# Kernel optimization log

Hardware: AMD Instinct MI355X
Metric: run time of the kernel (lower is better)

The kernel has to match this reference:

```python
import jax, jax.numpy as jnp
from jax import lax
import numpy as np

B, H, W = 8, 352, 1216
CLIPVARIANCE = 5.0   # init kwarg
MAXRANGE = 32        # init kwarg

# 1-pixel shifts with zero padding. out[...,m,n] = x at the shifted location.
def s_pos_w(x):  # out[..., n] = x[..., n-1]
    return jnp.pad(x[..., :, :-1], ((0, 0), (0, 0), (0, 0), (1, 0)))

def s_neg_w(x):  # out[..., n] = x[..., n+1]
    return jnp.pad(x[..., :, 1:], ((0, 0), (0, 0), (0, 0), (0, 1)))

def s_pos_h(x):  # out[..., m, :] = x[..., m-1, :]
    return jnp.pad(x[..., :-1, :], ((0, 0), (0, 0), (1, 0), (0, 0)))

def s_neg_h(x):  # out[..., m, :] = x[..., m+1, :]
    return jnp.pad(x[..., 1:, :], ((0, 0), (0, 0), (0, 1), (0, 0)))


def _dir_accumulate(shift, logstep, depthin, maskf, var_d):
    """Scan outward up to MAXRANGE steps in one direction, accumulating
    confidence weights exp(-min(var, clip)) and variance-weighted depth
    hypotheses depth[src] * exp(integrated log-gradient along the path).
    Paths break at the first unmasked pixel (valid is a running product)."""
    z = jnp.zeros_like(depthin)

    def body(carry, _):
        valid, c, dsh, vsh, aw, awd = carry
        valid = shift(valid * maskf)          # path contiguity
        c = logstep(c)                         # integrated log-depth ratio
        dsh = shift(dsh)                       # source-pixel depth
        vsh = shift(vsh)                       # source-pixel variance
        w = jnp.exp(-jnp.minimum(vsh, CLIPVARIANCE)) * valid
        aw = aw + w
        awd = awd + w * jnp.exp(c) * dsh
        return (valid, c, dsh, vsh, aw, awd), None

    init = (jnp.ones_like(depthin), z, depthin, var_d, z, z)
    (_, _, _, _, aw, awd), _ = lax.scan(body, init, None, length=MAXRANGE)
    return aw, awd


def crf_lateralre(pred_log, mask, variance, depthin):
    """One 4-direction variance-weighted CRF integration pass."""
    maskf = mask.astype(depthin.dtype)
    plog_h = pred_log[:, 0:1]  # log d[m,n+1] - log d[m,n]
    plog_v = pred_log[:, 1:2]  # log d[m+1,n] - log d[m,n]

    dirs = [
        (s_pos_w, lambda c: s_pos_w(c + plog_h), variance[:, 0:1]),  # from left
        (s_neg_w, lambda c: s_neg_w(c) - plog_h, variance[:, 1:2]),  # from right
        (s_pos_h, lambda c: s_pos_h(c + plog_v), variance[:, 2:3]),  # from above
        (s_neg_h, lambda c: s_neg_h(c) - plog_v, variance[:, 3:4]),  # from below
    ]

    tot_w = jnp.zeros_like(depthin)
    tot_wd = jnp.zeros_like(depthin)
    for shift, logstep, var_d in dirs:
        aw, awd = _dir_accumulate(shift, logstep, depthin, maskf, var_d)
        tot_w = tot_w + aw
        tot_wd = tot_wd + awd

    lateralre = jnp.where(tot_w > 0, tot_wd / jnp.maximum(tot_w, 1e-12), 0.0)
    return lateralre * maskf


def setup_inputs() -> dict:
    key = jax.random.key(0)
    k1, k2, k3, k4 = jax.random.split(key, 4)
    pred_log = jax.random.normal(k1, (B, 2, H, W), jnp.float32) * 0.05
    mask = (jax.random.uniform(k2, (B, 1, H, W)) < 0.9).astype(jnp.int32)
    variance = jax.random.uniform(k3, (B, 4, H, W), jnp.float32) * 8.0
    depthin = jax.random.uniform(k4, (B, 1, H, W), jnp.float32) * 10.0 + 1.0
    lam = jnp.array([0.2], jnp.float32)
    return {"pred_log": pred_log, "mask": mask, "variance": variance,
            "depthin": depthin, "lam": lam, "times": 1}


def reference(pred_log, mask, variance, depthin, lam, times):
    depthout = depthin
    for _ in range(times):
        lateralre = crf_lateralre(pred_log, mask, variance, depthout)
        sel = (lateralre > 0).astype(depthin.dtype)
        depthout = (1 - sel) * depthin + sel * (depthin * (1 - lam) + lateralre * lam)
    return depthout
```

## Files before the change

### kernel.cpp

```cpp
#include <hip/hip_runtime.h>
#include <stdint.h>

#define HH 352
#define WW 1216
#define HW (HH*WW)
#define BB 8
#define CLIPV 5.0f
#define MAXR 32

#define VR 22
#define NBAND (HH/VR)
#define PFD 12
#define TOT (VR + MAXR)

template<int DIR>
__device__ __forceinline__ void vert_scan(
    const int* __restrict__ m, const float* __restrict__ plog_v,
    const float* __restrict__ vp, const float* __restrict__ d,
    const int w, const int h0, const int lane,
    float2 (&obuf0)[VR][64], float (&obw)[VR], float (&obq)[VR])
{
    const int hs   = DIR ? (h0 + VR - 1 + MAXR) : (h0 - MAXR);
    const int step = DIR ? -1 : 1;

    float rq_q[VR], rq_w[VR];
    int   r_mi[PFD];
    float r_pl[PFD], r_vv[PFD], r_dd[PFD];

    #pragma unroll
    for (int p = 0; p < PFD; ++p) {
        int hp = hs + p * step;
        int hc = min(max(hp, 0), HH-1);
        int idx = hc * WW + w;
        r_mi[p] = m[idx];
        r_pl[p] = plog_v[idx];
        r_vv[p] = vp[idx];
        r_dd[p] = d[idx];
    }

    float Q = 0.f, W = 0.f, EG = 1.f;
    int last_inv = hs - step;

    #pragma unroll
    for (int it = 0; it < TOT; ++it) {
        const int h  = hs + it * step;
        const int sl = it % PFD;

        int   mi  = ((unsigned)h < (unsigned)HH) ? r_mi[sl] : 0;
        float pl  = r_pl[sl];
        float vvx = r_vv[sl];
        float dd  = r_dd[sl];

        if (it + PFD < TOT) {
            int hp = h + PFD * step;
            int hc = min(max(hp, 0), HH-1);
            int idx = hc * WW + w;
            r_mi[sl] = m[idx];
            r_pl[sl] = plog_v[idx];
            r_vv[sl] = vp[idx];
            r_dd[sl] = d[idx];
        }

        bool  res = (mi == 0);
        float g   = __expf(pl);
        float wt  = __expf(-fminf(vvx, CLIPV));
        float q, outw, outq;
        if constexpr (DIR == 0) {
            outw = W; outq = EG * Q;
            q = wt * dd * __builtin_amdgcn_rcpf(EG);
            Q  = res ? 0.f : (Q + q);
            W  = res ? 0.f : (W + wt);
            EG = res ? 1.f : (EG * g);
        } else {
            float EDh = EG * g;
            outw = W; outq = Q * __builtin_amdgcn_rcpf(EDh);
            q = wt * dd * EDh;
            Q  = res ? 0.f : (Q + q);
            W  = res ? 0.f : (W + wt);
            EG = res ? 1.f : EDh;
        }
        last_inv = res ? h : last_inv;

        if (it >= MAXR) {
            if constexpr (DIR == 0) obuf0[it - MAXR][lane] = make_float2(outw, outq);
            else { obw[VR - 1 - (it - MAXR)] = outw; obq[VR - 1 - (it - MAXR)] = outq; }
        }
        if (it < VR) { rq_q[it] = q; rq_w[it] = wt; }
        if (it >= MAXR) {
            int s_out = h - MAXR * step;
            bool alive = DIR ? (s_out < last_inv) : (s_out > last_inv);
            Q -= alive ? rq_q[it - MAXR] : 0.f;
            W -= alive ? rq_w[it - MAXR] : 0.f;
        }
    }
}

__global__ __launch_bounds__(128) void crf_vert(
    const float* __restrict__ pred_log, const int* __restrict__ mask,
    const float* __restrict__ variance, const float* __restrict__ depth,
    float2* __restrict__ vq)
{
    __shared__ float2 obuf0[VR][64];

    const int lane = threadIdx.x & 63;
    const int dir  = threadIdx.x >> 6;
    const int id   = blockIdx.x;
    const int xcd  = id & 7;
    const int seq  = id >> 3;
    const int wc   = seq % 19;
    const int t2   = seq / 19;
    const int band = xcd * 2 + (t2 & 1);
    const int b    = t2 >> 1;
    const int w    = wc * 64 + lane;

    const float* plog_v = pred_log + ((size_t)b*2 + 1) * HW;
    const int*   m  = mask     + (size_t)b*HW;
    const float* vp = variance + ((size_t)b*4 + (dir ? 3 : 2)) * HW;
    const float* d  = depth    + (size_t)b*HW;

    const int h0 = band * VR;

    float obw[VR], obq[VR];

    if (dir == 0) {
        vert_scan<0>(m, plog_v, vp, d, w, h0, lane, obuf0, obw, obq);
    } else {
        vert_scan<1>(m, plog_v, vp, d, w, h0, lane, obuf0, obw, obq);
    }

    __syncthreads();
    if (dir == 1) {
        float2* pvq = vq + (size_t)b*HW;
        const int w0 = wc * 64;
        #pragma unroll
        for (int r = 0; r < VR; ++r) {
            float2 a = obuf0[r][lane];
            pvq[(h0 + r) * WW + w0 + lane] = make_float2(a.x + obw[r], a.y + obq[r]);
        }
    }
}

__global__ __launch_bounds__(256) void crf_horiz(
    const float* __restrict__ pred_log, const int* __restrict__ mask,
    const float* __restrict__ variance, const float* __restrict__ depth,
    const float* __restrict__ lam_p,
    const float2* __restrict__ vq,
    float* __restrict__ out)
{
    __shared__ float sG[WW];
    __shared__ float sH[WW];
    __shared__ float sI[WW];
    __shared__ float sJ[WW];
    __shared__ float sEt[19], sEti[19], sTw0[19], sTq0[19];
    __shared__ unsigned long long sBal[19];

    const int tid  = threadIdx.x;
    const int lane = tid & 63;
    const int wv   = tid >> 6;
    const int i    = blockIdx.x;
    const int h    = (i & 7) * 44 + (i >> 3);
    const int b    = blockIdx.y;

    const float* plrow = pred_log + (size_t)b*2*HW + h*WW;
    const int*   mrow  = mask     + (size_t)b*HW   + h*WW;
    const float* v0row = variance + (size_t)b*4*HW + h*WW;
    const float* v1row = v0row + HW;
    const float* drow  = depth    + (size_t)b*HW   + h*WW;
    const float2* vqrow= vq  + (size_t)b*HW + h*WW;
    float*       orow  = out + (size_t)b*HW + h*WW;

    float l_pAx[5], l_xw0[5], l_xq0[5], l_iw1[5], l_iq1[5], l_m[5], l_d[5];

    #pragma unroll
    for (int r = 0; r < 5; ++r) {
        int c = r*4 + wv;
        if (c < 19) {
            int j = c*64 + lane;
            float pl  = plrow[j];
            int   mi  = mrow[j];
            float dj  = drow[j];
            float wt0 = __expf(-fminf(v0row[j], CLIPV));
            float wt1 = __expf(-fminf(v1row[j], CLIPV));
            float ipA = pl;
            #pragma unroll
            for (int dlt = 1; dlt < 64; dlt <<= 1) {
                float u = __shfl_up(ipA, dlt, 64);
                if (lane >= dlt) ipA += u;
            }
            float pAx = ipA - pl;
            float S   = __shfl(ipA, 63, 64);
            float Einv = __expf(-pAx);
            float q0 = wt0 * dj * Einv;
            float q1 = wt1 * dj * Einv;
            float iw0 = wt0, iq0 = q0, iw1 = wt1, iq1 = q1;
            #pragma unroll
            for (int dlt = 1; dlt < 64; dlt <<= 1) {
                float a = __shfl_up(iw0, dlt, 64);
                float e = __shfl_up(iq0, dlt, 64);
                float f = __shfl_up(iw1, dlt, 64);
                float g = __shfl_up(iq1, dlt, 64);
                if (lane >= dlt) { iw0 += a; iq0 += e; iw1 += f; iq1 += g; }
            }
            sG[j] = iw0 - wt0;
            sH[j] = iq0 - q0;
            sI[j] = iw1;
            sJ[j] = iq1;
            unsigned long long bal = __ballot(mi == 0);
            if (lane == 63) {
                sEt[c]  = __expf(S);
                sEti[c] = __expf(-S);
                sTw0[c] = iw0;
                sTq0[c] = iq0;
            }
            if (lane == 0) sBal[c] = bal;
            l_pAx[r] = pAx; l_xw0[r] = iw0 - wt0; l_xq0[r] = iq0 - q0;
            l_iw1[r] = iw1; l_iq1[r] = iq1;
            l_m[r] = (float)mi; l_d[r] = dj;
        }
    }
    __syncthreads();

    const float lam = lam_p[0];

    #pragma unroll
    for (int r = 0; r < 5; ++r) {
        int c = r*4 + wv;
        if (c < 19) {
            const int c0 = c*64;
            const int j  = c0 + lane;
            float E = __expf(l_pAx[r]);
            unsigned long long balOwn = sBal[c];
            unsigned long long mb = balOwn & ((1ull << lane) - 1ull);
            int lm = mb ? (c0 + 63 - __builtin_clzll(mb)) : -1;
            if (c > 0 && lane < 32) {
                unsigned long long mp = sBal[c-1] & ~((1ull << (lane + 32)) - 1ull);
                if (mp) { int lm2 = c0 - 64 + 63 - __builtin_clzll(mp); lm = max(lm, lm2); }
            }
            int a0 = max(j - MAXR, lm + 1);
            float W0, Q0;
            if (a0 >= c0) {
                W0 = l_xw0[r] - sG[a0];
                Q0 = E * (l_xq0[r] - sH[a0]);
            } else {
                W0 = l_xw0[r] + (sTw0[c-1] - sG[a0]);
                Q0 = E * l_xq0[r] + E * sEt[c-1] * (sTq0[c-1] - sH[a0]);
            }
            int nm = 1 << 30;
            if (lane < 63) {
                unsigned long long nb = balOwn >> (lane + 1);
                if (nb) nm = j + 1 + __builtin_ctzll(nb);
            }
            if (c < 18 && lane >= 32) {
                unsigned long long nn = sBal[c+1] & ((1ull << (lane - 31)) - 1ull);
                if (nn) nm = min(nm, c0 + 64 + (int)__builtin_ctzll(nn));
            }
            int b1 = min(j + MAXR, nm - 1);
            b1 = min(b1, WW - 1);
            int endin = min(b1, c0 + 63);
            float W1 = 0.f, Q1 = 0.f;
            if (endin > j) {
                W1 = sI[endin] - l_iw1[r];
                Q1 = E * (sJ[endin] - l_iq1[r]);
            }
            if (b1 > c0 + 63) {
                W1 += sI[b1];
                Q1 += E * sEti[c] * sJ[b1];
            }
            float2 vt = vqrow[j];
            float totw  = W0 + W1 + vt.x;
            float totwd = Q0 + Q1 + vt.y;
            float lat = (totw > 0.f) ? (totwd / fmaxf(totw, 1e-12f)) : 0.f;
            lat *= l_m[r];
            float dj = l_d[r];
            orow[j] = (lat > 0.f) ? (dj * (1.f - lam) + lat * lam) : dj;
        }
    }
}

#define BWF 256
#define PADF 32
#define LWF (BWF + 2*PADF)

__global__ __launch_bounds__(256) void crf_fallback(
    const float* __restrict__ pred_log, const int* __restrict__ mask,
    const float* __restrict__ variance, const float* __restrict__ depth,
    const float* __restrict__ lam_p, float* __restrict__ out)
{
    __shared__ float s_m[LWF], s_wt0[LWF], s_wt1[LWF], s_gh[LWF], s_ghi[LWF], s_d[LWF];
    const int t  = threadIdx.x;
    const int i  = blockIdx.x;
    const int h  = (i & 7) * 44 + (i >> 3);
    const int w0 = blockIdx.y * BWF;
    const int b  = blockIdx.z;
    const float* plog_h = pred_log + (size_t)b * 2 * HW;
    const float* plog_v = plog_h + HW;
    const int*   m      = mask   + (size_t)b * HW;
    const float* v0     = variance + (size_t)b * 4 * HW;
    const float* v1     = v0 + HW;
    const float* v2     = v0 + 2 * HW;
    const float* v3     = v0 + 3 * HW;
    const float* d      = depth + (size_t)b * HW;
    for (int j = t; j < LWF; j += BWF) {
        int gw = w0 - PADF + j;
        float mf=0.f, wt0=0.f, wt1=0.f, gh=1.f, ghi=1.f, dd=0.f;
        if (gw >= 0 && gw < WW) {
            int idx = h * WW + gw;
            mf = (float)m[idx];
            float pl = plog_h[idx];
            gh = __expf(pl); ghi = __expf(-pl);
            wt0 = __expf(-fminf(v0[idx], CLIPV));
            wt1 = __expf(-fminf(v1[idx], CLIPV));
            dd = d[idx];
        }
        s_m[j]=mf; s_wt0[j]=wt0; s_wt1[j]=wt1; s_gh[j]=gh; s_ghi[j]=ghi; s_d[j]=dd;
    }
    __syncthreads();
    const int w = w0 + t;
    if (w >= WW) return;
    const int c = t + PADF;
    float totw = 0.f, totwd = 0.f;
    { float e=1.f, valid=1.f;
      #pragma unroll 8
      for (int k=1;k<=MAXR;++k){int s=c-k; valid*=s_m[s]; e*=s_gh[s];
        float wgt=s_wt0[s]*valid; totw+=wgt; totwd+=wgt*e*s_d[s];} }
    { float e=1.f, valid=1.f;
      #pragma unroll 8
      for (int k=1;k<=MAXR;++k){int s=c+k; e*=s_ghi[s-1]; valid*=s_m[s];
        float wgt=s_wt1[s]*valid; totw+=wgt; totwd+=wgt*e*s_d[s];} }
    { const int kup=min(MAXR,h); float e=1.f, valid=1.f;
      #pragma unroll 4
      for (int k=1;k<=kup;++k){int idx=(h-k)*WW+w; valid*=(float)m[idx];
        e*=__expf(plog_v[idx]); float wgt=__expf(-fminf(v2[idx],CLIPV))*valid;
        totw+=wgt; totwd+=wgt*e*d[idx];} }
    { const int kdn=min(MAXR,HH-1-h); float e=1.f, valid=1.f;
      #pragma unroll 4
      for (int k=1;k<=kdn;++k){int idx=(h+k)*WW+w; e*=__expf(-plog_v[idx-WW]);
        valid*=(float)m[idx]; float wgt=__expf(-fminf(v3[idx],CLIPV))*valid;
        totw+=wgt; totwd+=wgt*e*d[idx];} }
    const int base = h * WW + w;
    float lat = (totw > 0.f) ? (totwd / fmaxf(totw, 1e-12f)) : 0.f;
    lat *= s_m[c];
    float lam = lam_p[0];
    float di  = s_d[c];
    out[(size_t)b * HW + base] = (lat > 0.f) ? (di * (1.f - lam) + lat * lam) : di;
}

extern "C" void kernel_launch(void* const* d_in, const int* in_sizes, int n_in,
                              void* d_out, int out_size, void* d_ws, size_t ws_size,
                              hipStream_t stream) {
    const float* pred_log = (const float*)d_in[0];
    const int*   mask     = (const int*)  d_in[1];
    const float* variance = (const float*)d_in[2];
    const float* depthin  = (const float*)d_in[3];
    const float* lam      = (const float*)d_in[4];
    float* out = (float*)d_out;

    const size_t need = (size_t)BB * HW * sizeof(float2);
    if (ws_size >= need) {
        float2* vq = (float2*)d_ws;
        dim3 vgrid(19 * NBAND * BB, 1, 1);
        hipLaunchKernelGGL(crf_vert, vgrid, dim3(128), 0, stream,
                           pred_log, mask, variance, depthin, vq);
        dim3 hgrid(HH, BB);
        hipLaunchKernelGGL(crf_horiz, hgrid, dim3(256), 0, stream,
                           pred_log, mask, variance, depthin, lam, vq, out);
    } else {
        dim3 fgrid(HH, (WW + BWF - 1) / BWF, BB);
        hipLaunchKernelGGL(crf_fallback, fgrid, dim3(BWF), 0, stream,
                           pred_log, mask, variance, depthin, lam, out);
    }
}
```

Measured before the change: 184.2 us.

## Drop manual register prefetch and stage both vertical scans in shared memory

Removes the hand-rolled 12-deep register prefetch ring in the vertical scan and loads each row directly, leaving scheduling to the compiler under full unrolling. Both scan directions now write their outputs to separate shared buffers instead of keeping one direction in registers. Both warps then split the combine-and-store rows, so the final write work is spread over the two wavefronts. The aim is to cut register pressure and balance the epilogue, at the cost of more LDS use and possibly less explicit latency hiding on global loads.

```diff
diff --git a/kernel.cpp b/kernel.cpp
--- a/kernel.cpp
+++ b/kernel.cpp
@@ -10,7 +10,6 @@
 
 #define VR 22
 #define NBAND (HH/VR)
-#define PFD 12
 #define TOT (VR + MAXR)
 
 template<int DIR>
@@ -18,25 +17,12 @@
     const int* __restrict__ m, const float* __restrict__ plog_v,
     const float* __restrict__ vp, const float* __restrict__ d,
     const int w, const int h0, const int lane,
-    float2 (&obuf0)[VR][64], float (&obw)[VR], float (&obq)[VR])
+    float2 (&obuf)[VR][64])
 {
     const int hs   = DIR ? (h0 + VR - 1 + MAXR) : (h0 - MAXR);
     const int step = DIR ? -1 : 1;
 
     float rq_q[VR], rq_w[VR];
-    int   r_mi[PFD];
-    float r_pl[PFD], r_vv[PFD], r_dd[PFD];
-
-    #pragma unroll
-    for (int p = 0; p < PFD; ++p) {
-        int hp = hs + p * step;
-        int hc = min(max(hp, 0), HH-1);
-        int idx = hc * WW + w;
-        r_mi[p] = m[idx];
-        r_pl[p] = plog_v[idx];
-        r_vv[p] = vp[idx];
-        r_dd[p] = d[idx];
-    }
 
     float Q = 0.f, W = 0.f, EG = 1.f;
     int last_inv = hs - step;
@@ -44,22 +30,13 @@
     #pragma unroll
     for (int it = 0; it < TOT; ++it) {
         const int h  = hs + it * step;
-        const int sl = it % PFD;
-
-        int   mi  = ((unsigned)h < (unsigned)HH) ? r_mi[sl] : 0;
-        float pl  = r_pl[sl];
-        float vvx = r_vv[sl];
-        float dd  = r_dd[sl];
-
-        if (it + PFD < TOT) {
-            int hp = h + PFD * step;
-            int hc = min(max(hp, 0), HH-1);
-            int idx = hc * WW + w;
-            r_mi[sl] = m[idx];
-            r_pl[sl] = plog_v[idx];
-            r_vv[sl] = vp[idx];
-            r_dd[sl] = d[idx];
-        }
+        const int hc = min(max(h, 0), HH-1);
+        const int idx = hc * WW + w;
+
+        int   mi  = ((unsigned)h < (unsigned)HH) ? m[idx] : 0;
+        float pl  = plog_v[idx];
+        float vvx = vp[idx];
+        float dd  = d[idx];
 
         bool  res = (mi == 0);
         float g   = __expf(pl);
@@ -82,8 +59,8 @@
         last_inv = res ? h : last_inv;
 
         if (it >= MAXR) {
-            if constexpr (DIR == 0) obuf0[it - MAXR][lane] = make_float2(outw, outq);
-            else { obw[VR - 1 - (it - MAXR)] = outw; obq[VR - 1 - (it - MAXR)] = outq; }
+            const int r = DIR ? (VR - 1 - (it - MAXR)) : (it - MAXR);
+            obuf[r][lane] = make_float2(outw, outq);
         }
         if (it < VR) { rq_q[it] = q; rq_w[it] = wt; }
         if (it >= MAXR) {
@@ -100,7 +77,8 @@
     const float* __restrict__ variance, const float* __restrict__ depth,
     float2* __restrict__ vq)
 {
-    __shared__ float2 obuf0[VR][64];
+    __shared__ float2 obufA[VR][64];
+    __shared__ float2 obufB[VR][64];
 
     const int lane = threadIdx.x & 63;
     const int dir  = threadIdx.x >> 6;
@@ -120,22 +98,23 @@
 
     const int h0 = band * VR;
 
-    float obw[VR], obq[VR];
-
     if (dir == 0) {
-        vert_scan<0>(m, plog_v, vp, d, w, h0, lane, obuf0, obw, obq);
+        vert_scan<0>(m, plog_v, vp, d, w, h0, lane, obufA);
     } else {
-        vert_scan<1>(m, plog_v, vp, d, w, h0, lane, obuf0, obw, obq);
+        vert_scan<1>(m, plog_v, vp, d, w, h0, lane, obufB);
     }
 
     __syncthreads();
-    if (dir == 1) {
+    {
         float2* pvq = vq + (size_t)b*HW;
-        const int w0 = wc * 64;
+        const int w0c = wc * 64;
+        const int rbeg = dir ? (VR/2) : 0;
+        const int rend = dir ? VR : (VR/2);
         #pragma unroll
-        for (int r = 0; r < VR; ++r) {
-            float2 a = obuf0[r][lane];
-            pvq[(h0 + r) * WW + w0 + lane] = make_float2(a.x + obw[r], a.y + obq[r]);
+        for (int r = rbeg; r < rend; ++r) {
+            float2 a = obufA[r][lane];
+            float2 c = obufB[r][lane];
+            pvq[(h0 + r) * WW + w0c + lane] = make_float2(a.x + c.x, a.y + c.y);
         }
     }
 }
```

Measured after the change: 201.6 us. 9.4% more time.
